# Kernel optimization log

Measured on AMD Instinct MI355X. Metric: run time of the kernel, lower is better.

The kernel has to match this reference:

```python
import jax, jax.numpy as jnp
import numpy as np

N_NODES = 50000
N_EDGES = 800000
N_GRAPHS = 64
NEG_SLOPE = 0.2  # PyG GATConv default leaky_relu slope
EPS = 1e-16      # PyG softmax denominator epsilon


def gat_conv(x, W, a_src, a_dst, bias, src, dst, n_nodes):
    """PyG GATConv (heads=1, concat=True, self-loops already appended).
    x: [N, F_in], W: [F_in, H*F], a_src/a_dst: [H, F], bias: [H*F]."""
    H, F = a_src.shape
    h = (x @ W).reshape(-1, H, F)                      # [N, H, F]
    alpha_src = jnp.einsum('nhf,hf->nh', h, a_src)     # [N, H]
    alpha_dst = jnp.einsum('nhf,hf->nh', h, a_dst)     # [N, H]
    e = jax.nn.leaky_relu(alpha_src[src] + alpha_dst[dst], NEG_SLOPE)  # [E, H]
    # segment softmax over incoming edges of each destination node
    e_max = jax.ops.segment_max(e, dst, num_segments=n_nodes)          # [N, H]
    e_exp = jnp.exp(e - e_max[dst])
    denom = jax.ops.segment_sum(e_exp, dst, num_segments=n_nodes)      # [N, H]
    alpha = e_exp / (denom[dst] + EPS)                                 # [E, H]
    msg = alpha[:, :, None] * h[src]                                   # [E, H, F]
    out = jax.ops.segment_sum(msg, dst, num_segments=n_nodes)          # [N, H, F]
    return out.reshape(-1, H * F) + bias


def global_mean_pool(x, batch, n_graphs):
    s = jax.ops.segment_sum(x, batch, num_segments=n_graphs)
    cnt = jax.ops.segment_sum(jnp.ones((x.shape[0],), x.dtype), batch, num_segments=n_graphs)
    return s / jnp.maximum(cnt, 1.0)[:, None]


def setup_inputs() -> dict:
    key = jax.random.key(0)
    ks = jax.random.split(key, 10)
    d_in, d_h, d_out, L, H = 128, 128, 10, 3, 1
    x = jax.random.normal(ks[0], (N_NODES, d_in), dtype=jnp.float32)
    edge_index = jax.random.randint(ks[1], (2, N_EDGES), 0, N_NODES, dtype=jnp.int32)
    edge_attr = jax.random.normal(ks[2], (N_EDGES, 4), dtype=jnp.float32)
    batch = jnp.sort(jax.random.randint(ks[3], (N_NODES,), 0, N_GRAPHS, dtype=jnp.int32))
    s0 = 1.0 / np.sqrt(d_in)
    sh = 1.0 / np.sqrt(d_h)
    return {
        'x': x,
        'edge_index': edge_index,
        'edge_attr': edge_attr,
        'batch': batch,
        'W0': jax.random.normal(ks[4], (d_in, d_h), dtype=jnp.float32) * s0,
        'b0': jnp.zeros((d_h,), jnp.float32),
        'Wc': jax.random.normal(ks[5], (L, d_h, H * d_h), dtype=jnp.float32) * sh,
        'att_src': jax.random.normal(ks[6], (L, H, d_h), dtype=jnp.float32) * sh,
        'att_dst': jax.random.normal(ks[7], (L, H, d_h), dtype=jnp.float32) * sh,
        'bc': jnp.zeros((L, H * d_h), jnp.float32),
        'W1': jax.random.normal(ks[8], (d_h, d_out), dtype=jnp.float32) * sh,
        'b1': jnp.zeros((d_out,), jnp.float32),
    }


def reference(x, edge_index, edge_attr, batch, W0, b0, Wc, att_src, att_dst, bc, W1, b1):
    n = x.shape[0]
    # GATConv default add_self_loops=True
    loops = jnp.arange(n, dtype=edge_index.dtype)
    src = jnp.concatenate([edge_index[0], loops])
    dst = jnp.concatenate([edge_index[1], loops])
    # dropout p=0 / eval mode -> identity
    h = jax.nn.relu(x @ W0 + b0)
    for i in range(Wc.shape[0]):
        h = jax.nn.relu(gat_conv(h, Wc[i], att_src[i], att_dst[i], bc[i], src, dst, n))
    pooled = global_mean_pool(h, batch, N_GRAPHS)   # [B, d_h]
    return pooled @ W1 + b1                          # [B, d_out]
```

## Files before the change

kernel.cpp:

```cpp
#include <hip/hip_runtime.h>
#include <hip/hip_bf16.h>
#include <hip/hip_fp16.h>
#include <hip/hip_fp8.h>

#define NN 50000
#define NE 800000
#define NG 64
#define DH 128

#define NPB 256
#define NBK ((NN + NPB - 1) / NPB)
#define EPB 4096
#define NPBLK ((NE + EPB - 1) / EPB)
#define CAPB 5120
#define GEMMB 782
#define CST 136
#define CSTB 136
#define SMEM_BYTES 18432

#if defined(__has_builtin)
# if __has_builtin(__builtin_amdgcn_cvt_pk_f32_fp8) && __has_builtin(__builtin_amdgcn_cvt_pk_fp8_f32)
#  define HW_FP8 1
# endif
#endif

typedef __bf16 bfx8 __attribute__((ext_vector_type(8)));
typedef float  f32x4 __attribute__((ext_vector_type(4)));

__device__ __forceinline__ ushort f2b(float f) {
    unsigned b = __float_as_uint(f);
    b += 0x7fff + ((b >> 16) & 1);
    return (ushort)(b >> 16);
}
__device__ __forceinline__ float b2f(ushort s) {
    return __uint_as_float((unsigned)s << 16);
}
__device__ __forceinline__ unsigned pk2(float a, float b) {
    return (unsigned)f2b(a) | ((unsigned)f2b(b) << 16);
}
__device__ __forceinline__ unsigned f2fp8(float v) {
    v = fminf(fmaxf(v, -448.f), 448.f);
#ifdef HW_FP8
    return (unsigned)__builtin_amdgcn_cvt_pk_fp8_f32(v, v, 0, false) & 0xFFu;
#else
    __hip_fp8_e4m3 t(v);
    return (unsigned)*(const unsigned char*)&t;
#endif
}
__device__ __forceinline__ void fp8x4_up(unsigned u, float* o) {
#ifdef HW_FP8
    auto lo = __builtin_amdgcn_cvt_pk_f32_fp8((int)u, false);
    auto hi = __builtin_amdgcn_cvt_pk_f32_fp8((int)u, true);
    o[0] = lo[0]; o[1] = lo[1]; o[2] = hi[0]; o[3] = hi[1];
#else
    #pragma unroll
    for (int k = 0; k < 4; ++k) {
        unsigned char c = (u >> (8 * k)) & 0xFF;
        o[k] = float(*(const __hip_fp8_e4m3*)&c);
    }
#endif
}

__launch_bounds__(256)
__global__ void k_partwt(const int* __restrict__ ei, int* __restrict__ gcur,
                         unsigned* __restrict__ tmp,
                         const float* __restrict__ W0, const float* __restrict__ Wc,
                         ushort* __restrict__ Wt) {
    int t = threadIdx.x;
    if (blockIdx.x >= NPBLK) {
        int i = (blockIdx.x - NPBLK) * 256 + t;
        int m = i >> 14;
        int r = i & 16383;
        int k = r >> 7, n = r & 127;
        const float* src = (m == 0) ? W0 : (Wc + (size_t)(m - 1) * DH * DH);
        Wt[(size_t)m * DH * DH + n * DH + k] = f2b(src[r]);
        return;
    }
    __shared__ int cnt[NBK], base[NBK], lcur[NBK];
    for (int i = t; i < NBK; i += 256) cnt[i] = 0;
    __syncthreads();
    int e0 = blockIdx.x * EPB;
    int dreg[16];
    #pragma unroll
    for (int j = 0; j < 16; ++j) {
        int e = e0 + j * 256 + t;
        dreg[j] = (e < NE) ? ei[NE + e] : -1;
        if (e < NE) atomicAdd(&cnt[dreg[j] >> 8], 1);
    }
    __syncthreads();
    for (int i = t; i < NBK; i += 256) {
        base[i] = cnt[i] ? atomicAdd(&gcur[i], cnt[i]) : 0;
        lcur[i] = 0;
    }
    __syncthreads();
    #pragma unroll
    for (int j = 0; j < 16; ++j) {
        int e = e0 + j * 256 + t;
        if (e < NE) {
            int d = dreg[j], s = ei[e];
            int b = d >> 8;
            int r = atomicAdd(&lcur[b], 1);
            tmp[(size_t)b * CAPB + base[b] + r] = ((unsigned)(d & 255) << 16) | (unsigned)s;
        }
    }
}

__launch_bounds__(256)
__global__ void k_bcount(const unsigned* __restrict__ tmp, const int* __restrict__ gcur,
                         int* __restrict__ deg, int* __restrict__ ploc,
                         int* __restrict__ bsizeP) {
    __shared__ int dcnt[NPB];
    int b = blockIdx.x, t = threadIdx.x;
    dcnt[t] = 0;
    __syncthreads();
    int ne = gcur[b];
    for (int e = t; e < ne; e += 256)
        atomicAdd(&dcnt[tmp[(size_t)b * CAPB + e] >> 16], 1);
    __syncthreads();
    int n = b * NPB + t;
    int d = (n < NN) ? dcnt[t] : 0;
    int p = (n < NN) ? ((d + 4) & ~3) : 0;
    int inc = p;
    #pragma unroll
    for (int off = 1; off < 64; off <<= 1) {
        int u = __shfl_up(inc, off);
        if ((t & 63) >= off) inc += u;
    }
    __shared__ int wsum[4];
    if ((t & 63) == 63) wsum[t >> 6] = inc;
    __syncthreads();
    int w = t >> 6, woff = 0;
    #pragma unroll
    for (int k = 0; k < 4; ++k) if (k < w) woff += wsum[k];
    int lofs = inc - p + woff;
    if (n < NN) { deg[n] = d; ploc[n] = lofs; }
    if (t == 255) bsizeP[b] = lofs + p;
}

template<bool AF32, bool DOTS, bool OUTFP8>
__device__ __forceinline__ void gemm_body(char* smem, int gblk,
        const void* __restrict__ Av, const ushort* __restrict__ Wt,
        const float* __restrict__ bias, void* __restrict__ C, int relu,
        const float* __restrict__ avs, const float* __restrict__ avd,
        float* __restrict__ asrc, float* __restrict__ adst) {
    int tid = threadIdx.x;
    int wid = (gblk * 256 + tid) >> 6;
    int lane = tid & 63;
    int row0 = wid * 16;
    if (row0 >= NN) return;
    int mrow = lane & 15;
    int quad = lane >> 4;
    int arow = row0 + mrow;

    f32x4 acc[8];
    #pragma unroll
    for (int t = 0; t < 8; ++t)
        #pragma unroll
        for (int r = 0; r < 4; ++r) acc[t][r] = 0.f;

    #pragma unroll
    for (int ks = 0; ks < 4; ++ks) {
        int k0 = ks * 32 + quad * 8;
        bfx8 a;
        if (AF32) {
            const float* ap = (const float*)Av + (size_t)arow * DH + k0;
            union { ushort s[8]; bfx8 v; } u;
            #pragma unroll
            for (int j = 0; j < 8; ++j) u.s[j] = f2b(ap[j]);
            a = u.v;
        } else {
            a = *(const bfx8*)((const ushort*)Av + (size_t)arow * DH + k0);
        }
        #pragma unroll
        for (int t = 0; t < 8; ++t) {
            bfx8 b = *(const bfx8*)(Wt + (size_t)(t * 16 + mrow) * DH + k0);
            acc[t] = __builtin_amdgcn_mfma_f32_16x16x32_bf16(a, b, acc[t], 0, 0, 0);
        }
    }

    if (OUTFP8) {
        uchar* my = (uchar*)smem + (tid >> 6) * 16 * CSTB;
        #pragma unroll
        for (int t = 0; t < 8; ++t) {
            int col = t * 16 + mrow;
            float bv = bias ? bias[col] : 0.f;
            #pragma unroll
            for (int r = 0; r < 4; ++r) {
                float v = acc[t][r] + bv;
                if (relu) v = fmaxf(v, 0.f);
                my[(quad * 4 + r) * CSTB + col] = (uchar)f2fp8(v);
            }
        }
        #pragma unroll
        for (int i = 0; i < 4; ++i) {
            int idx = i * 64 + lane;
            int row = idx >> 4;
            int c8 = idx & 15;
            uint2 u = *(const uint2*)(my + row * CSTB + c8 * 8);
            *(uint2*)((uchar*)C + (size_t)(row0 + row) * DH + c8 * 8) = u;
        }
    } else {
        ushort* my = (ushort*)smem + (tid >> 6) * 16 * CST;
        #pragma unroll
        for (int t = 0; t < 8; ++t) {
            int col = t * 16 + mrow;
            float bv = bias ? bias[col] : 0.f;
            #pragma unroll
            for (int r = 0; r < 4; ++r) {
                float v = acc[t][r] + bv;
                if (relu) v = fmaxf(v, 0.f);
                my[(quad * 4 + r) * CST + col] = f2b(v);
            }
        }
        #pragma unroll
        for (int i = 0; i < 4; ++i) {
            int idx = i * 64 + lane;
            int row = idx >> 4;
            int c16 = idx & 15;
            uint4 u = *(const uint4*)(my + row * CST + c16 * 8);
            *(uint4*)((ushort*)C + (size_t)(row0 + row) * DH + c16 * 8) = u;
        }
    }

    if (DOTS) {
        float av[8], dv[8];
        #pragma unroll
        for (int t = 0; t < 8; ++t) {
            av[t] = avs[t * 16 + mrow];
            dv[t] = avd[t * 16 + mrow];
        }
        int orow = row0 + quad * 4;
        #pragma unroll
        for (int r = 0; r < 4; ++r) {
            float ps = 0.f, pd = 0.f;
            #pragma unroll
            for (int t = 0; t < 8; ++t) {
                ps += acc[t][r] * av[t];
                pd += acc[t][r] * dv[t];
            }
            #pragma unroll
            for (int off = 1; off < 16; off <<= 1) {
                ps += __shfl_xor(ps, off);
                pd += __shfl_xor(pd, off);
            }
            if (mrow == 0) {
                asrc[orow + r] = ps;
                adst[orow + r] = pd;
            }
        }
    }
}

__launch_bounds__(256)
__global__ void k_buildgemm(const unsigned* __restrict__ tmp, const int* __restrict__ gcur,
                            const int* __restrict__ bsizeP, const int* __restrict__ ploc,
                            int* __restrict__ pstart, ushort* __restrict__ csr,
                            const float* __restrict__ x, const ushort* __restrict__ Wt,
                            const float* __restrict__ b0, ushort* __restrict__ hB) {
    __shared__ char smem[SMEM_BYTES];
    int t = threadIdx.x;
    if (blockIdx.x < GEMMB) {
        gemm_body<true, false, false>(smem, blockIdx.x, x, Wt, b0, hB, 1,
                                      nullptr, nullptr, nullptr, nullptr);
        return;
    }
    int b = blockIdx.x - GEMMB;
    ushort* buf = (ushort*)smem;
    int* lcur = (int*)(smem + 16384);
    int* sm   = (int*)(smem + 16384 + 1024);
    int v = (t < NBK) ? bsizeP[t] : 0;
    sm[t] = v;
    __syncthreads();
    for (int off = 1; off < 256; off <<= 1) {
        int u = (t >= off) ? sm[t - off] : 0;
        __syncthreads();
        sm[t] += u;
        __syncthreads();
    }
    int r0 = sm[b] - bsizeP[b];
    int S = bsizeP[b];
    int n0 = b * NPB, n1 = min(n0 + NPB, NN), nodes = n1 - n0;
    int ne = gcur[b];

    if (S <= 8192) {
        for (int i = t; i < (S >> 1); i += 256) ((unsigned*)buf)[i] = 0;
        __syncthreads();
        if (t < nodes) {
            int lp = ploc[n0 + t];
            pstart[n0 + t] = r0 + lp;
            lcur[t] = lp + 1;
            buf[lp] = (ushort)(n0 + t);
        }
        __syncthreads();
        for (int e = t; e < ne; e += 256) {
            unsigned u = tmp[(size_t)b * CAPB + e];
            int slot = atomicAdd(&lcur[u >> 16], 1);
            buf[slot] = (ushort)(u & 0xffffu);
        }
        __syncthreads();
        unsigned* dst = (unsigned*)(csr + r0);
        for (int i = t; i < (S >> 1); i += 256) dst[i] = ((unsigned*)buf)[i];
    } else {
        for (int i = t; i < S; i += 256) csr[r0 + i] = 0;
        __syncthreads();
        if (t < nodes) {
            int lp = ploc[n0 + t];
            pstart[n0 + t] = r0 + lp;
            lcur[t] = r0 + lp + 1;
            csr[r0 + lp] = (ushort)(n0 + t);
        }
        __syncthreads();
        for (int e = t; e < ne; e += 256) {
            unsigned u = tmp[(size_t)b * CAPB + e];
            int slot = atomicAdd(&lcur[u >> 16], 1);
            csr[slot] = (ushort)(u & 0xffffu);
        }
    }
}

__launch_bounds__(256)
__global__ void k_gemmdots(const ushort* __restrict__ hB, const ushort* __restrict__ Wt,
                           uchar* __restrict__ hA,
                           const float* __restrict__ avs, const float* __restrict__ avd,
                           float* __restrict__ asrc, float* __restrict__ adst) {
    __shared__ char smem[SMEM_BYTES];
    gemm_body<false, true, true>(smem, blockIdx.x, hB, Wt, nullptr, hA, 0,
                                 avs, avd, asrc, adst);
}

__launch_bounds__(256)
__global__ void k_aggr(const uchar* __restrict__ h8, const float* __restrict__ asrc,
                       const float* __restrict__ adst, const int* __restrict__ pstart,
                       const int* __restrict__ deg, const ushort* __restrict__ csr,
                       const float* __restrict__ bias, ushort* __restrict__ hout) {
    int wid = (blockIdx.x * blockDim.x + threadIdx.x) >> 6;
    int lane = threadIdx.x & 63;
    if (wid >= NN) return;
    int start = pstart[wid];
    int cnt = deg[wid] + 1;
    float ad = adst[wid];

    if (cnt <= 64) {
        int s = csr[start + lane];
        float e = -1e30f;
        if (lane < cnt) {
            float t = asrc[s] + ad;
            e = fmaxf(t, 0.f) + 0.2f * fminf(t, 0.f);
        }
        float m = e;
        #pragma unroll
        for (int off = 32; off; off >>= 1) m = fmaxf(m, __shfl_xor(m, off));
        float w = (lane < cnt) ? __expf(e - m) : 0.f;
        float dsum = w;
        #pragma unroll
        for (int off = 32; off; off >>= 1) dsum += __shfl_xor(dsum, off);

        int g = lane >> 4, fidx = lane & 15;
        float acc[8];
        #pragma unroll
        for (int k = 0; k < 8; ++k) acc[k] = 0.f;

        int steps = (cnt + 3) >> 2;
        const uint2* hp = (const uint2*)h8;
        int j = 0;
        for (; j + 3 < steps; j += 4) {
            int   e0 = j * 4 + g,      e1 = e0 + 4,  e2 = e0 + 8,  e3 = e0 + 12;
            float w0 = __shfl(w, e0),  w1 = __shfl(w, e1);
            float w2 = __shfl(w, e2),  w3 = __shfl(w, e3);
            int   s0 = __shfl(s, e0),  s1 = __shfl(s, e1);
            int   s2 = __shfl(s, e2),  s3 = __shfl(s, e3);
            uint2 u0 = hp[(size_t)s0 * 16 + fidx];
            uint2 u1 = hp[(size_t)s1 * 16 + fidx];
            uint2 u2 = hp[(size_t)s2 * 16 + fidx];
            uint2 u3 = hp[(size_t)s3 * 16 + fidx];
            float v[8];
            fp8x4_up(u0.x, v); fp8x4_up(u0.y, v + 4);
            #pragma unroll
            for (int k = 0; k < 8; ++k) acc[k] += w0 * v[k];
            fp8x4_up(u1.x, v); fp8x4_up(u1.y, v + 4);
            #pragma unroll
            for (int k = 0; k < 8; ++k) acc[k] += w1 * v[k];
            fp8x4_up(u2.x, v); fp8x4_up(u2.y, v + 4);
            #pragma unroll
            for (int k = 0; k < 8; ++k) acc[k] += w2 * v[k];
            fp8x4_up(u3.x, v); fp8x4_up(u3.y, v + 4);
            #pragma unroll
            for (int k = 0; k < 8; ++k) acc[k] += w3 * v[k];
        }
        for (; j < steps; ++j) {
            int e0 = j * 4 + g;
            float w0 = __shfl(w, e0);
            int   s0 = __shfl(s, e0);
            uint2 u0 = hp[(size_t)s0 * 16 + fidx];
            float v[8];
            fp8x4_up(u0.x, v); fp8x4_up(u0.y, v + 4);
            #pragma unroll
            for (int k = 0; k < 8; ++k) acc[k] += w0 * v[k];
        }
        #pragma unroll
        for (int k = 0; k < 8; ++k) {
            acc[k] += __shfl_xor(acc[k], 16);
            acc[k] += __shfl_xor(acc[k], 32);
        }
        if (g == 0) {
            float inv = 1.f / (dsum + 1e-16f);
            const float4* bp = (const float4*)bias;
            float4 b0 = bp[fidx * 2], b1 = bp[fidx * 2 + 1];
            uint4 o;
            o.x = pk2(fmaxf(acc[0] * inv + b0.x, 0.f), fmaxf(acc[1] * inv + b0.y, 0.f));
            o.y = pk2(fmaxf(acc[2] * inv + b0.z, 0.f), fmaxf(acc[3] * inv + b0.w, 0.f));
            o.z = pk2(fmaxf(acc[4] * inv + b1.x, 0.f), fmaxf(acc[5] * inv + b1.y, 0.f));
            o.w = pk2(fmaxf(acc[6] * inv + b1.z, 0.f), fmaxf(acc[7] * inv + b1.w, 0.f));
            ((uint4*)hout)[(size_t)wid * 16 + fidx] = o;
        }
        return;
    }

    float m = -1e30f;
    for (int i0 = start; i0 < start + cnt; i0 += 64) {
        int i = i0 + lane;
        float e = -1e30f;
        if (i < start + cnt) {
            int s = csr[i];
            float t = asrc[s] + ad;
            e = fmaxf(t, 0.f) + 0.2f * fminf(t, 0.f);
        }
        m = fmaxf(m, e);
    }
    #pragma unroll
    for (int off = 32; off; off >>= 1) m = fmaxf(m, __shfl_xor(m, off));

    float accx = 0.f, accy = 0.f, dsum = 0.f;
    for (int i0 = start; i0 < start + cnt; i0 += 64) {
        int i = i0 + lane;
        int s = 0; float w = 0.f;
        if (i < start + cnt) {
            s = csr[i];
            float t = asrc[s] + ad;
            float e = fmaxf(t, 0.f) + 0.2f * fminf(t, 0.f);
            w = __expf(e - m);
        }
        dsum += w;
        int cl = min(64, start + cnt - i0);
        for (int j = 0; j < cl; ++j) {
            int   sj = __shfl(s, j);
            float wj = __shfl(w, j);
            unsigned us = *(const ushort*)(h8 + (size_t)sj * DH + lane * 2);
            float v[4];
            fp8x4_up(us, v);
            accx += wj * v[0];
            accy += wj * v[1];
        }
    }
    #pragma unroll
    for (int off = 32; off; off >>= 1) dsum += __shfl_xor(dsum, off);

    float inv = 1.f / (dsum + 1e-16f);
    float ox = fmaxf(accx * inv + bias[lane * 2], 0.f);
    float oy = fmaxf(accy * inv + bias[lane * 2 + 1], 0.f);
    *(unsigned*)(hout + (size_t)wid * DH + lane * 2) = pk2(ox, oy);
}

__launch_bounds__(256)
__global__ void k_pool(const ushort* __restrict__ h, const int* __restrict__ batch,
                       float* __restrict__ gsum, int* __restrict__ gcnt) {
    int slot = threadIdx.x >> 7;
    int f = threadIdx.x & 127;
    int n0 = blockIdx.x * 64;
    int n1 = min(n0 + 64, NN);
    int first = n0 + slot;
    if (first >= n1) return;
    int g0 = batch[n0], g1 = batch[n1 - 1];
    if (g0 == g1) {
        float acc = 0.f;
        for (int nd = first; nd < n1; nd += 2)
            acc += b2f(h[(size_t)nd * DH + f]);
        atomicAdd(&gsum[g0 * DH + f], acc);
        if (f == 0 && slot == 0) atomicAdd(&gcnt[g0], n1 - n0);
        return;
    }
    float acc = 0.f; int run = 0;
    int gcur = batch[first];
    for (int nd = first; nd < n1; nd += 2) {
        int g = batch[nd];
        if (g != gcur) {
            atomicAdd(&gsum[gcur * DH + f], acc);
            if (f == 0) atomicAdd(&gcnt[gcur], run);
            acc = 0.f; run = 0; gcur = g;
        }
        acc += b2f(h[(size_t)nd * DH + f]);
        run += 1;
    }
    atomicAdd(&gsum[gcur * DH + f], acc);
    if (f == 0) atomicAdd(&gcnt[gcur], run);
}

__global__ void k_final(const float* __restrict__ gsum, const int* __restrict__ gcnt,
                        const float* __restrict__ W1, const float* __restrict__ b1,
                        float* __restrict__ out) {
    int t = threadIdx.x;
    if (t >= NG * 10) return;
    int g = t / 10, o = t % 10;
    float inv = 1.f / fmaxf((float)gcnt[g], 1.f);
    float acc = 0.f;
    for (int f = 0; f < DH; ++f) acc += gsum[g * DH + f] * W1[f * 10 + o];
    out[t] = acc * inv + b1[o];
}

extern "C" void kernel_launch(void* const* d_in, const int* in_sizes, int n_in,
                              void* d_out, int out_size, void* d_ws, size_t ws_size,
                              hipStream_t stream) {
    const float* x       = (const float*)d_in[0];
    const int*   ei      = (const int*)d_in[1];
    const int*   batch   = (const int*)d_in[3];
    const float* W0      = (const float*)d_in[4];
    const float* b0      = (const float*)d_in[5];
    const float* Wc      = (const float*)d_in[6];
    const float* att_src = (const float*)d_in[7];
    const float* att_dst = (const float*)d_in[8];
    const float* bc      = (const float*)d_in[9];
    const float* W1      = (const float*)d_in[10];
    const float* b1      = (const float*)d_in[11];
    float* out = (float*)d_out;

    char* ws = (char*)d_ws;
    size_t off = 0;
    auto alloc = [&](size_t bytes) {
        void* p = ws + off;
        off += (bytes + 255) & ~(size_t)255;
        return p;
    };
    uchar*    hA     = (uchar*)alloc((size_t)NN * DH);
    ushort*   hB     = (ushort*)alloc((size_t)NN * DH * 2);
    ushort*   Wt     = (ushort*)alloc((size_t)4 * DH * DH * 2);
    int*      pstart = (int*)alloc((size_t)NN * 4);
    ushort*   csr    = (ushort*)alloc((size_t)(NE + 4 * NN + 64) * 2);
    unsigned* tmp    = (unsigned*)alloc((size_t)NBK * CAPB * 4);
    float*    asrc   = (float*)alloc(NN * 4);
    float*    adst   = (float*)alloc(NN * 4);
    int*      deg    = (int*)alloc(NN * 4);
    int*      ploc   = (int*)alloc(NN * 4);
    int*      gcur   = (int*)alloc((NBK + 1) * 4);
    int*      bsizeP = (int*)alloc((NBK + 1) * 4);
    float*    gsum   = (float*)alloc(NG * DH * 4);
    int*      gcnt   = (int*)alloc(NG * 4);

    hipMemsetAsync(gcur, 0, (NBK + 1) * 4, stream);
    hipMemsetAsync(gsum, 0, NG * DH * 4 + 256, stream);

    k_partwt<<<NPBLK + 256, 256, 0, stream>>>(ei, gcur, tmp, W0, Wc, Wt);
    k_bcount<<<NBK, 256, 0, stream>>>(tmp, gcur, deg, ploc, bsizeP);
    k_buildgemm<<<GEMMB + NBK, 256, 0, stream>>>(tmp, gcur, bsizeP, ploc, pstart, csr,
                                                 x, Wt, b0, hB);

    for (int l = 0; l < 3; ++l) {
        k_gemmdots<<<GEMMB, 256, 0, stream>>>(hB, Wt + (size_t)(l + 1) * DH * DH, hA,
                                              att_src + l * DH, att_dst + l * DH,
                                              asrc, adst);
        k_aggr<<<(NN + 3) / 4, 256, 0, stream>>>(hA, asrc, adst, pstart, deg, csr,
                                                 bc + l * DH, hB);
    }

    k_pool<<<(NN + 63) / 64, 256, 0, stream>>>(hB, batch, gsum, gcnt);
    k_final<<<1, NG * 10, 0, stream>>>(gsum, gcnt, W1, b1, out);
}
```

Measured before the change: 327.1 us.

## Fuse global mean pool into last GAT aggregation via atomics

Removes the separate pooling kernel. The final aggregation layer now atomically adds each node's post-ReLU features straight into per-graph sums instead of writing the hidden state. Per-graph node counting moves into the bucket-count kernel, and the two memsets are merged into one by reordering workspace allocations. The trade-off is millions of fp32 global atomics spread over only 64×128 addresses, which can cause heavy contention in exchange for skipping one write and one read of the hidden state.

```diff
diff --git a/kernel.cpp b/kernel.cpp
--- a/kernel.cpp
+++ b/kernel.cpp
@@ -108,7 +108,8 @@
 __launch_bounds__(256)
 __global__ void k_bcount(const unsigned* __restrict__ tmp, const int* __restrict__ gcur,
                          int* __restrict__ deg, int* __restrict__ ploc,
-                         int* __restrict__ bsizeP) {
+                         int* __restrict__ bsizeP, const int* __restrict__ batch,
+                         int* __restrict__ gcnt) {
     __shared__ int dcnt[NPB];
     int b = blockIdx.x, t = threadIdx.x;
     dcnt[t] = 0;
@@ -118,6 +119,7 @@
         atomicAdd(&dcnt[tmp[(size_t)b * CAPB + e] >> 16], 1);
     __syncthreads();
     int n = b * NPB + t;
+    if (n < NN) atomicAdd(&gcnt[batch[n]], 1);
     int d = (n < NN) ? dcnt[t] : 0;
     int p = (n < NN) ? ((d + 4) & ~3) : 0;
     int inc = p;
@@ -328,11 +330,13 @@
                                  avs, avd, asrc, adst);
 }
 
+template<bool POOL>
 __launch_bounds__(256)
 __global__ void k_aggr(const uchar* __restrict__ h8, const float* __restrict__ asrc,
                        const float* __restrict__ adst, const int* __restrict__ pstart,
                        const int* __restrict__ deg, const ushort* __restrict__ csr,
-                       const float* __restrict__ bias, ushort* __restrict__ hout) {
+                       const float* __restrict__ bias, ushort* __restrict__ hout,
+                       const int* __restrict__ batch, float* __restrict__ gsum) {
     int wid = (blockIdx.x * blockDim.x + threadIdx.x) >> 6;
     int lane = threadIdx.x & 63;
     if (wid >= NN) return;
@@ -406,12 +410,28 @@
             float inv = 1.f / (dsum + 1e-16f);
             const float4* bp = (const float4*)bias;
             float4 b0 = bp[fidx * 2], b1 = bp[fidx * 2 + 1];
-            uint4 o;
-            o.x = pk2(fmaxf(acc[0] * inv + b0.x, 0.f), fmaxf(acc[1] * inv + b0.y, 0.f));
-            o.y = pk2(fmaxf(acc[2] * inv + b0.z, 0.f), fmaxf(acc[3] * inv + b0.w, 0.f));
-            o.z = pk2(fmaxf(acc[4] * inv + b1.x, 0.f), fmaxf(acc[5] * inv + b1.y, 0.f));
-            o.w = pk2(fmaxf(acc[6] * inv + b1.z, 0.f), fmaxf(acc[7] * inv + b1.w, 0.f));
-            ((uint4*)hout)[(size_t)wid * 16 + fidx] = o;
+            float vv[8];
+            vv[0] = fmaxf(acc[0] * inv + b0.x, 0.f);
+            vv[1] = fmaxf(acc[1] * inv + b0.y, 0.f);
+            vv[2] = fmaxf(acc[2] * inv + b0.z, 0.f);
+            vv[3] = fmaxf(acc[3] * inv + b0.w, 0.f);
+            vv[4] = fmaxf(acc[4] * inv + b1.x, 0.f);
+            vv[5] = fmaxf(acc[5] * inv + b1.y, 0.f);
+            vv[6] = fmaxf(acc[6] * inv + b1.z, 0.f);
+            vv[7] = fmaxf(acc[7] * inv + b1.w, 0.f);
+            if (POOL) {
+                int gg = batch[wid];
+                float* gp = gsum + (size_t)gg * DH + fidx * 8;
+                #pragma unroll
+                for (int k = 0; k < 8; ++k) atomicAdd(&gp[k], vv[k]);
+            } else {
+                uint4 o;
+                o.x = pk2(vv[0], vv[1]);
+                o.y = pk2(vv[2], vv[3]);
+                o.z = pk2(vv[4], vv[5]);
+                o.w = pk2(vv[6], vv[7]);
+                ((uint4*)hout)[(size_t)wid * 16 + fidx] = o;
+            }
         }
         return;
     }
@@ -458,41 +478,13 @@
     float inv = 1.f / (dsum + 1e-16f);
     float ox = fmaxf(accx * inv + bias[lane * 2], 0.f);
     float oy = fmaxf(accy * inv + bias[lane * 2 + 1], 0.f);
-    *(unsigned*)(hout + (size_t)wid * DH + lane * 2) = pk2(ox, oy);
-}
-
-__launch_bounds__(256)
-__global__ void k_pool(const ushort* __restrict__ h, const int* __restrict__ batch,
-                       float* __restrict__ gsum, int* __restrict__ gcnt) {
-    int slot = threadIdx.x >> 7;
-    int f = threadIdx.x & 127;
-    int n0 = blockIdx.x * 64;
-    int n1 = min(n0 + 64, NN);
-    int first = n0 + slot;
-    if (first >= n1) return;
-    int g0 = batch[n0], g1 = batch[n1 - 1];
-    if (g0 == g1) {
-        float acc = 0.f;
-        for (int nd = first; nd < n1; nd += 2)
-            acc += b2f(h[(size_t)nd * DH + f]);
-        atomicAdd(&gsum[g0 * DH + f], acc);
-        if (f == 0 && slot == 0) atomicAdd(&gcnt[g0], n1 - n0);
-        return;
-    }
-    float acc = 0.f; int run = 0;
-    int gcur = batch[first];
-    for (int nd = first; nd < n1; nd += 2) {
-        int g = batch[nd];
-        if (g != gcur) {
-            atomicAdd(&gsum[gcur * DH + f], acc);
-            if (f == 0) atomicAdd(&gcnt[gcur], run);
-            acc = 0.f; run = 0; gcur = g;
-        }
-        acc += b2f(h[(size_t)nd * DH + f]);
-        run += 1;
-    }
-    atomicAdd(&gsum[gcur * DH + f], acc);
-    if (f == 0) atomicAdd(&gcnt[gcur], run);
+    if (POOL) {
+        int gg = batch[wid];
+        atomicAdd(&gsum[(size_t)gg * DH + lane * 2], ox);
+        atomicAdd(&gsum[(size_t)gg * DH + lane * 2 + 1], oy);
+    } else {
+        *(unsigned*)(hout + (size_t)wid * DH + lane * 2) = pk2(ox, oy);
+    }
 }
 
 __global__ void k_final(const float* __restrict__ gsum, const int* __restrict__ gcnt,
@@ -540,16 +532,15 @@
     float*    adst   = (float*)alloc(NN * 4);
     int*      deg    = (int*)alloc(NN * 4);
     int*      ploc   = (int*)alloc(NN * 4);
-    int*      gcur   = (int*)alloc((NBK + 1) * 4);
     int*      bsizeP = (int*)alloc((NBK + 1) * 4);
     float*    gsum   = (float*)alloc(NG * DH * 4);
     int*      gcnt   = (int*)alloc(NG * 4);
-
-    hipMemsetAsync(gcur, 0, (NBK + 1) * 4, stream);
-    hipMemsetAsync(gsum, 0, NG * DH * 4 + 256, stream);
+    int*      gcur   = (int*)alloc((NBK + 1) * 4);
+
+    hipMemsetAsync(gsum, 0, NG * DH * 4 + 256 + 1024, stream);
 
     k_partwt<<<NPBLK + 256, 256, 0, stream>>>(ei, gcur, tmp, W0, Wc, Wt);
-    k_bcount<<<NBK, 256, 0, stream>>>(tmp, gcur, deg, ploc, bsizeP);
+    k_bcount<<<NBK, 256, 0, stream>>>(tmp, gcur, deg, ploc, bsizeP, batch, gcnt);
     k_buildgemm<<<GEMMB + NBK, 256, 0, stream>>>(tmp, gcur, bsizeP, ploc, pstart, csr,
                                                  x, Wt, b0, hB);
 
@@ -557,10 +548,13 @@
         k_gemmdots<<<GEMMB, 256, 0, stream>>>(hB, Wt + (size_t)(l + 1) * DH * DH, hA,
                                               att_src + l * DH, att_dst + l * DH,
                                               asrc, adst);
-        k_aggr<<<(NN + 3) / 4, 256, 0, stream>>>(hA, asrc, adst, pstart, deg, csr,
-                                                 bc + l * DH, hB);
-    }
-
-    k_pool<<<(NN + 63) / 64, 256, 0, stream>>>(hB, batch, gsum, gcnt);
+        if (l < 2)
+            k_aggr<false><<<(NN + 3) / 4, 256, 0, stream>>>(
+                hA, asrc, adst, pstart, deg, csr, bc + l * DH, hB, nullptr, nullptr);
+        else
+            k_aggr<true><<<(NN + 3) / 4, 256, 0, stream>>>(
+                hA, asrc, adst, pstart, deg, csr, bc + l * DH, nullptr, batch, gsum);
+    }
+
     k_final<<<1, NG * 10, 0, stream>>>(gsum, gcnt, W1, b1, out);
 }
```

Result: slower. 1.025 ms (+213.3%).
